# Performance work log

Hardware: AMD Instinct MI355X
Metric: run time of the kernel (lower is better)

Reference implementation:

```python
import jax, jax.numpy as jnp
import numpy as np

N, E, D_IN, D_HID, D_OUT = 50000, 800000, 128, 128, 128


def setup_inputs() -> dict:
    key = jax.random.key(0)
    ks = jax.random.split(key, 10)
    x = jax.random.normal(ks[0], (N, D_IN), dtype=jnp.float32)
    edge_index = jax.random.randint(ks[1], (2, E), 0, N, dtype=jnp.int64)
    def xavier(k, fan_in, fan_out):
        lim = jnp.sqrt(6.0 / (fan_in + fan_out)).astype(jnp.float32)
        return jax.random.uniform(k, (fan_in, fan_out), jnp.float32, -lim, lim)
    return {
        "x": x,
        "edge_index": edge_index,
        "W1l": xavier(ks[2], D_IN, D_HID), "b1l": jnp.zeros((D_HID,), jnp.float32),
        "W1r": xavier(ks[3], D_IN, D_HID),
        "W2l": xavier(ks[4], D_HID, D_OUT), "b2l": jnp.zeros((D_OUT,), jnp.float32),
        "W2r": xavier(ks[5], D_HID, D_OUT),
        "Wfc": xavier(ks[6], D_OUT, 2), "bfc": jnp.zeros((2,), jnp.float32),
    }


def _mean_aggregate(x, src, dst, num_nodes):
    # gather neighbor (source) features, scatter-mean to destination nodes
    msgs = x[src]                                        # [E, D]
    summed = jax.ops.segment_sum(msgs, dst, num_segments=num_nodes)
    ones = jnp.ones((src.shape[0],), x.dtype)
    counts = jax.ops.segment_sum(ones, dst, num_segments=num_nodes)
    return summed / jnp.maximum(counts, 1.0)[:, None]


def _l2_normalize(x, eps=1e-12):
    # matches torch F.normalize(p=2, dim=-1): divide by clamp(norm, min=eps)
    norm = jnp.sqrt(jnp.sum(x * x, axis=-1, keepdims=True))
    return x / jnp.maximum(norm, eps)


def _sage_conv(x, src, dst, Wl, bl, Wr):
    agg = _mean_aggregate(x, src, dst, x.shape[0])
    out = agg @ Wl + bl + x @ Wr
    return _l2_normalize(out)


def reference(x, edge_index, W1l, b1l, W1r, W2l, b2l, W2r, Wfc, bfc):
    src, dst = edge_index[0], edge_index[1]  # PyG: row=source(j), col=target(i)
    h = _sage_conv(x, src, dst, W1l, b1l, W1r)
    h = jax.nn.relu(h)
    h = _sage_conv(h, src, dst, W2l, b2l, W2r)
    logits = h @ Wfc + bfc
    return jax.nn.softmax(logits, axis=-1)
```

## Files before the change

### kernel.cpp

```cpp
#include <hip/hip_runtime.h>

#define D 128
#define CBITS 8

typedef __attribute__((ext_vector_type(8))) short short8;
typedef __attribute__((ext_vector_type(4))) float f32x4;

__device__ __forceinline__ unsigned short f2b(float f) {
    unsigned u = __builtin_bit_cast(unsigned, f);
    u += 0x7fffu + ((u >> 16) & 1u);
    return (unsigned short)(u >> 16);
}
__device__ __forceinline__ float b2f(unsigned short b) {
    unsigned u = ((unsigned)b) << 16;
    return __builtin_bit_cast(float, u);
}


__global__ __launch_bounds__(256) void prep_kernel(
    const float* __restrict__ x, unsigned short* __restrict__ acat,
    unsigned char* __restrict__ xq8, int nCast, int n8,
    const float* __restrict__ W1l, const float* __restrict__ W1r,
    const float* __restrict__ W2l, const float* __restrict__ W2r,
    unsigned short* __restrict__ WT1, unsigned short* __restrict__ WT2,
    int4* __restrict__ zeroPtr, int* __restrict__ offsets, int nnodes, int E) {
    const int b = blockIdx.x;
    const int t = threadIdx.x;
    if (b < nCast) {
        int g = b * 256 + t;
        if (g < n8) {
            int row = g >> 4, chunk = g & 15;
            const float4 v0 = *reinterpret_cast<const float4*>(x + (size_t)g * 8);
            const float4 v1 = *reinterpret_cast<const float4*>(x + (size_t)g * 8 + 4);
            float f[8] = {v0.x, v0.y, v0.z, v0.w, v1.x, v1.y, v1.z, v1.w};
            short8 r;
            unsigned lo = 0, hi = 0;
#pragma unroll
            for (int i = 0; i < 8; ++i) {
                r[i] = (short)f2b(f[i]);
                int qi = (int)rintf(fminf(fmaxf(f[i] * 32.f, -127.f), 127.f)) + 128;
                if (i < 4) lo |= (unsigned)(qi & 255) << (8 * i);
                else       hi |= (unsigned)(qi & 255) << (8 * (i - 4));
            }
            *reinterpret_cast<short8*>(acat + (size_t)row * 256 + 128 + chunk * 8) = r;
            *reinterpret_cast<uint2*>(xq8 + (size_t)row * 128 + chunk * 8) = make_uint2(lo, hi);
        }
    } else if (b < nCast + 256) {
        int bb = b - nCast;
        int layer = bb >> 7;
        int j = bb & 127;
        const float* Wl = layer ? W2l : W1l;
        const float* Wr = layer ? W2r : W1r;
        unsigned short* WT = layer ? WT2 : WT1;
        float v = (t < 128) ? Wl[t * D + j] : Wr[(t - 128) * D + j];
        WT[(size_t)j * 256 + t] = f2b(v);
    } else {
        if (t < 128) zeroPtr[t] = make_int4(0, 0, 0, 0);
        if (t == 0) offsets[nnodes] = E;
    }
}


__global__ __launch_bounds__(256) void bucket_count_kernel(
    const int* __restrict__ dst, int* __restrict__ bucketCnt, int E) {
    __shared__ int hist[256];
    const int t = threadIdx.x;
    hist[t] = 0;
    __syncthreads();
    const int base = blockIdx.x * 4096;
#pragma unroll
    for (int i = 0; i < 16; ++i) {
        int e = base + i * 256 + t;
        if (e < E) atomicAdd(&hist[dst[e] >> CBITS], 1);
    }
    __syncthreads();
    if (hist[t]) atomicAdd(&bucketCnt[t], hist[t]);
}

__global__ __launch_bounds__(256) void bin_coarse_kernel(
    const int* __restrict__ src, const int* __restrict__ dst,
    const int* __restrict__ bucketCnt, int* __restrict__ cursorA,
    int* __restrict__ staging, int E) {

    __shared__ int hist[256];
    __shared__ int lcur[256];
    const int t = threadIdx.x;

    int cnt = bucketCnt[t];
    lcur[t] = cnt;
    __syncthreads();
    for (int d = 1; d < 256; d <<= 1) {
        int u = (t >= d) ? lcur[t - d] : 0;
        __syncthreads();
        lcur[t] += u;
        __syncthreads();
    }
    const int myBase = lcur[t] - cnt;
    __syncthreads();

    hist[t] = 0;
    __syncthreads();

    const int base = blockIdx.x * 4096;
    int sreg[16], dreg[16];
#pragma unroll
    for (int i = 0; i < 16; ++i) {
        int e = base + i * 256 + t;
        int s = 0, d = -1;
        if (e < E) {
            s = src[e]; d = dst[e];
            atomicAdd(&hist[d >> CBITS], 1);
        }
        sreg[i] = s; dreg[i] = d;
    }
    __syncthreads();
    {
        int h = hist[t];
        lcur[t] = myBase + (h ? atomicAdd(&cursorA[t], h) : 0);
    }
    __syncthreads();
#pragma unroll
    for (int i = 0; i < 16; ++i) {
        if (dreg[i] >= 0) {
            int p = atomicAdd(&lcur[dreg[i] >> CBITS], 1);
            staging[p] = sreg[i] | ((dreg[i] & 255) << 16);
        }
    }
}

__global__ __launch_bounds__(256) void bucket_build_kernel(
    const int* __restrict__ staging, const int* __restrict__ bucketCnt,
    int* __restrict__ offsets, unsigned short* __restrict__ csr, int nnodes) {

    __shared__ int A1[256];
    __shared__ int A2[256];
    const int t = threadIdx.x;
    const int b = blockIdx.x;

    int cnt = bucketCnt[t];
    A1[t] = cnt;
    __syncthreads();
    for (int d = 1; d < 256; d <<= 1) {
        int u = (t >= d) ? A1[t - d] : 0;
        __syncthreads();
        A1[t] += u;
        __syncthreads();
    }
    const int end  = A1[b];
    const int base = end - bucketCnt[b];
    __syncthreads();

    A1[t] = 0;
    __syncthreads();
    for (int i = base + t; i < end; i += 256)
        atomicAdd(&A1[(staging[i] >> 16) & 255], 1);
    __syncthreads();
    A2[t] = A1[t];
    __syncthreads();
    for (int d = 1; d < 256; d <<= 1) {
        int u = (t >= d) ? A2[t - d] : 0;
        __syncthreads();
        A2[t] += u;
        __syncthreads();
    }
    const int excl = A2[t] - A1[t];
    const int node = (b << CBITS) + t;
    if (node < nnodes) offsets[node] = base + excl;
    __syncthreads();
    A1[t] = base + excl;
    __syncthreads();
    for (int i = base + t; i < end; i += 256) {
        int p = staging[i];
        int c = atomicAdd(&A1[(p >> 16) & 255], 1);
        csr[c] = (unsigned short)(p & 0xFFFF);
    }
}


__global__ __launch_bounds__(256) void aggregate_kernel(
    const unsigned char* __restrict__ q8,
    const int* __restrict__ offsets, const unsigned short* __restrict__ csr,
    unsigned short* __restrict__ out,
    int nnodes, float invScale) {
    int node = blockIdx.x * 16 + (threadIdx.x >> 4);
    int l16 = threadIdx.x & 15;
    if (node >= nnodes) return;
    const int lo = offsets[node], hi = offsets[node + 1];
    const int deg = hi - lo;
    const unsigned M = 0x00FF00FFu;
    unsigned a0 = 0, a1 = 0, a2 = 0, a3 = 0;
    int k = lo;
    int kA = (lo + 7) & ~7; if (kA > hi) kA = hi;
    for (; k < kA; ++k) {
        int s = csr[k];
        const uint2 v = *reinterpret_cast<const uint2*>(q8 + (size_t)s * 128 + l16 * 8);
        a0 += v.x & M; a1 += (v.x >> 8) & M;
        a2 += v.y & M; a3 += (v.y >> 8) & M;
    }
    for (; k + 8 <= hi; k += 8) {
        const int4 c = *reinterpret_cast<const int4*>(csr + k);
        int s[8];
        s[0] = c.x & 0xFFFF; s[1] = (int)((unsigned)c.x >> 16);
        s[2] = c.y & 0xFFFF; s[3] = (int)((unsigned)c.y >> 16);
        s[4] = c.z & 0xFFFF; s[5] = (int)((unsigned)c.z >> 16);
        s[6] = c.w & 0xFFFF; s[7] = (int)((unsigned)c.w >> 16);
        uint2 v[8];
#pragma unroll
        for (int u = 0; u < 8; ++u)
            v[u] = *reinterpret_cast<const uint2*>(q8 + (size_t)s[u] * 128 + l16 * 8);
#pragma unroll
        for (int u = 0; u < 8; ++u) {
            a0 += v[u].x & M; a1 += (v[u].x >> 8) & M;
            a2 += v[u].y & M; a3 += (v[u].y >> 8) & M;
        }
    }
    for (; k < hi; ++k) {
        int s = csr[k];
        const uint2 v = *reinterpret_cast<const uint2*>(q8 + (size_t)s * 128 + l16 * 8);
        a0 += v.x & M; a1 += (v.x >> 8) & M;
        a2 += v.y & M; a3 += (v.y >> 8) & M;
    }
    const float inv = invScale / fmaxf((float)deg, 1.0f);
    const float bias = 128.0f * (float)deg;
    int isum[8];
    isum[0] = (int)(a0 & 0xFFFF); isum[2] = (int)(a0 >> 16);
    isum[1] = (int)(a1 & 0xFFFF); isum[3] = (int)(a1 >> 16);
    isum[4] = (int)(a2 & 0xFFFF); isum[6] = (int)(a2 >> 16);
    isum[5] = (int)(a3 & 0xFFFF); isum[7] = (int)(a3 >> 16);
    short8 r;
#pragma unroll
    for (int i = 0; i < 8; ++i) r[i] = (short)f2b(((float)isum[i] - bias) * inv);
    *reinterpret_cast<short8*>(out + (size_t)node * 256 + l16 * 8) = r;
}


template <bool RELU, bool HEAD>
__global__ __launch_bounds__(256) void sage_mfma_kernel(
    const unsigned short* __restrict__ Acat, const unsigned short* __restrict__ WT,
    const float* __restrict__ bias, unsigned short* __restrict__ hout, int out_stride,
    unsigned char* __restrict__ q8out,
    const float* __restrict__ Wfc, const float* __restrict__ bfc,
    float* __restrict__ outf, int nnodes) {

    __shared__ unsigned short Blds[128 * 256];
    const int tid = threadIdx.x;

    {
        const short8* wsrc = reinterpret_cast<const short8*>(WT);
#pragma unroll
        for (int it = 0; it < 16; ++it) {
            int u = it * 256 + tid;
            int row = u >> 5, c = u & 31;
            int cs = c ^ (row & 7);
            *reinterpret_cast<short8*>(
                reinterpret_cast<char*>(Blds) + row * 512 + cs * 16) = wsrc[u];
        }
    }
    __syncthreads();

    const int w = tid >> 6, l = tid & 63;
    const int r16 = l & 15, g = l >> 4;
    const int rowbase = blockIdx.x * 128 + w * 32;

    f32x4 acc[2][8];
#pragma unroll
    for (int j = 0; j < 8; ++j) {
        float bj = bias[j * 16 + r16];
        acc[0][j] = (f32x4){bj, bj, bj, bj};
        acc[1][j] = (f32x4){bj, bj, bj, bj};
    }

    const unsigned short* ap0 = Acat + (size_t)(rowbase + r16) * 256 + g * 8;
    const unsigned short* ap1 = ap0 + 16 * 256;

#pragma unroll
    for (int ks = 0; ks < 8; ++ks) {
        const short8 a0 = *reinterpret_cast<const short8*>(ap0 + ks * 32);
        const short8 a1 = *reinterpret_cast<const short8*>(ap1 + ks * 32);
        const int cs = ((ks * 4 + g) ^ (r16 & 7)) * 16;
#pragma unroll
        for (int j = 0; j < 8; ++j) {
            const short8 b = *reinterpret_cast<const short8*>(
                reinterpret_cast<const char*>(Blds) + (j * 16 + r16) * 512 + cs);
            acc[0][j] = __builtin_amdgcn_mfma_f32_16x16x32_bf16(a0, b, acc[0][j], 0, 0, 0);
            acc[1][j] = __builtin_amdgcn_mfma_f32_16x16x32_bf16(a1, b, acc[1][j], 0, 0, 0);
        }
    }

#pragma unroll
    for (int rb = 0; rb < 2; ++rb) {
        float ss[4] = {0.f, 0.f, 0.f, 0.f};
#pragma unroll
        for (int j = 0; j < 8; ++j)
#pragma unroll
            for (int i = 0; i < 4; ++i) ss[i] += acc[rb][j][i] * acc[rb][j][i];
#pragma unroll
        for (int m = 1; m < 16; m <<= 1)
#pragma unroll
            for (int i = 0; i < 4; ++i) ss[i] += __shfl_xor(ss[i], m, 64);

        if (!HEAD) {
#pragma unroll
            for (int i = 0; i < 4; ++i) {
                int row = rowbase + rb * 16 + g * 4 + i;
                if (row >= nnodes) continue;
                float sc = 1.0f / fmaxf(sqrtf(ss[i]), 1e-12f);
#pragma unroll
                for (int j = 0; j < 8; ++j) {
                    float v = acc[rb][j][i] * sc;
                    if (RELU) v = fmaxf(v, 0.f);
                    hout[(size_t)row * out_stride + j * 16 + r16] = f2b(v);
                    if (RELU)
                        q8out[(size_t)row * 128 + j * 16 + r16] =
                            (unsigned char)((int)rintf(v * 127.f) + 128);
                }
            }
        } else {
            float w0[8], w1[8];
#pragma unroll
            for (int j = 0; j < 8; ++j) {
                const float2 wv = *reinterpret_cast<const float2*>(Wfc + (j * 16 + r16) * 2);
                w0[j] = wv.x; w1[j] = wv.y;
            }
            const float b0 = bfc[0], b1 = bfc[1];
#pragma unroll
            for (int i = 0; i < 4; ++i) {
                float sc = 1.0f / fmaxf(sqrtf(ss[i]), 1e-12f);
                float l0 = 0.f, l1 = 0.f;
#pragma unroll
                for (int j = 0; j < 8; ++j) {
                    float v = acc[rb][j][i] * sc;
                    l0 = fmaf(v, w0[j], l0);
                    l1 = fmaf(v, w1[j], l1);
                }
#pragma unroll
                for (int m = 1; m < 16; m <<= 1) {
                    l0 += __shfl_xor(l0, m, 64);
                    l1 += __shfl_xor(l1, m, 64);
                }
                int row = rowbase + rb * 16 + g * 4 + i;
                if (r16 == 0 && row < nnodes) {
                    float d0 = l0 + b0, d1 = l1 + b1;
                    float mx = fmaxf(d0, d1);
                    float e0 = expf(d0 - mx), e1 = expf(d1 - mx);
                    float inv = 1.0f / (e0 + e1);
                    outf[(size_t)row * 2]     = e0 * inv;
                    outf[(size_t)row * 2 + 1] = e1 * inv;
                }
            }
        }
    }
}


extern "C" void kernel_launch(void* const* d_in, const int* in_sizes, int n_in,
                              void* d_out, int out_size, void* d_ws, size_t ws_size,
                              hipStream_t stream) {
    const float* x   = (const float*)d_in[0];
    const int*   ei  = (const int*)d_in[1];
    const float* W1l = (const float*)d_in[2];
    const float* b1l = (const float*)d_in[3];
    const float* W1r = (const float*)d_in[4];
    const float* W2l = (const float*)d_in[5];
    const float* b2l = (const float*)d_in[6];
    const float* W2r = (const float*)d_in[7];
    const float* Wfc = (const float*)d_in[8];
    const float* bfc = (const float*)d_in[9];

    const int N = in_sizes[0] / D;
    const int E = in_sizes[1] / 2;
    const int* src = ei;
    const int* dst = ei + E;
    const int NBC = (N + (1 << CBITS) - 1) >> CBITS;

    unsigned short* Acat1 = (unsigned short*)d_ws;
    unsigned short* Acat2 = Acat1 + (size_t)N * 256;
    int* staging          = (int*)Acat2;
    unsigned short* WT1   = Acat2 + (size_t)N * 256;
    unsigned short* WT2   = WT1 + 128 * 256;
    int* bucketCnt  = (int*)(WT2 + 128 * 256);
    int* cursorA    = bucketCnt + 256;
    unsigned char* q8 = (unsigned char*)(cursorA + 256);
    int* offsets    = (int*)(q8 + (size_t)N * 128);
    unsigned short* csr = (unsigned short*)(((uintptr_t)(offsets + N + 1) + 15) & ~(uintptr_t)15);

    const int nCast = (N * 16 + 255) / 256;

    prep_kernel<<<nCast + 256 + 1, 256, 0, stream>>>(
        x, Acat1, q8, nCast, N * 16, W1l, W1r, W2l, W2r, WT1, WT2,
        (int4*)bucketCnt, offsets, N, E);

    bucket_count_kernel<<<(E + 4095) / 4096, 256, 0, stream>>>(dst, bucketCnt, E);
    bin_coarse_kernel<<<(E + 4095) / 4096, 256, 0, stream>>>(src, dst, bucketCnt, cursorA, staging, E);
    bucket_build_kernel<<<NBC, 256, 0, stream>>>(staging, bucketCnt, offsets, csr, N);

    aggregate_kernel<<<(N + 15) / 16, 256, 0, stream>>>(q8, offsets, csr, Acat1, N, 1.0f / 32.0f);
    sage_mfma_kernel<true, false><<<(N + 127) / 128, 256, 0, stream>>>(
        Acat1, WT1, b1l, Acat2 + 128, 256, q8, nullptr, nullptr, nullptr, N);

    aggregate_kernel<<<(N + 15) / 16, 256, 0, stream>>>(q8, offsets, csr, Acat2, N, 1.0f / 127.0f);
    sage_mfma_kernel<false, true><<<(N + 127) / 128, 256, 0, stream>>>(
        Acat2, WT2, b2l, nullptr, 0, nullptr, Wfc, bfc, (float*)d_out, N);
}
```

Measured before the change: 112.6 us.

## Split int8 feature table into two column halves for cache-friendly gathers

Stores the quantized int8 node features as two separate 64-column halves, each covering all nodes, and has the aggregation kernel process one half per block, with 8 lanes per node. Each half-table is 3.2 MB instead of 6.4 MB, so the random neighbor gathers of a given half are more likely to hit in L2. The trade-off is that the CSR indices and offsets are read twice, and more blocks are launched with smaller per-node work.

```diff
diff --git a/kernel.cpp b/kernel.cpp
--- a/kernel.cpp
+++ b/kernel.cpp
@@ -43,7 +43,9 @@
                 else       hi |= (unsigned)(qi & 255) << (8 * (i - 4));
             }
             *reinterpret_cast<short8*>(acat + (size_t)row * 256 + 128 + chunk * 8) = r;
-            *reinterpret_cast<uint2*>(xq8 + (size_t)row * 128 + chunk * 8) = make_uint2(lo, hi);
+            int half = chunk >> 3;
+            *reinterpret_cast<uint2*>(xq8 + (size_t)half * nnodes * 64 +
+                                      (size_t)row * 64 + (chunk & 7) * 8) = make_uint2(lo, hi);
         }
     } else if (b < nCast + 256) {
         int bb = b - nCast;
@@ -181,10 +183,13 @@
     const unsigned char* __restrict__ q8,
     const int* __restrict__ offsets, const unsigned short* __restrict__ csr,
     unsigned short* __restrict__ out,
-    int nnodes, float invScale) {
-    int node = blockIdx.x * 16 + (threadIdx.x >> 4);
-    int l16 = threadIdx.x & 15;
+    int nnodes, float invScale, int nodeBlocks) {
+    const int h  = blockIdx.x / nodeBlocks;
+    const int nb = blockIdx.x - h * nodeBlocks;
+    const int node = nb * 32 + (threadIdx.x >> 3);
+    const int l8 = threadIdx.x & 7;
     if (node >= nnodes) return;
+    const unsigned char* slice = q8 + (size_t)h * nnodes * 64;
     const int lo = offsets[node], hi = offsets[node + 1];
     const int deg = hi - lo;
     const unsigned M = 0x00FF00FFu;
@@ -193,7 +198,7 @@
     int kA = (lo + 7) & ~7; if (kA > hi) kA = hi;
     for (; k < kA; ++k) {
         int s = csr[k];
-        const uint2 v = *reinterpret_cast<const uint2*>(q8 + (size_t)s * 128 + l16 * 8);
+        const uint2 v = *reinterpret_cast<const uint2*>(slice + (size_t)s * 64 + l8 * 8);
         a0 += v.x & M; a1 += (v.x >> 8) & M;
         a2 += v.y & M; a3 += (v.y >> 8) & M;
     }
@@ -207,7 +212,7 @@
         uint2 v[8];
 #pragma unroll
         for (int u = 0; u < 8; ++u)
-            v[u] = *reinterpret_cast<const uint2*>(q8 + (size_t)s[u] * 128 + l16 * 8);
+            v[u] = *reinterpret_cast<const uint2*>(slice + (size_t)s[u] * 64 + l8 * 8);
 #pragma unroll
         for (int u = 0; u < 8; ++u) {
             a0 += v[u].x & M; a1 += (v[u].x >> 8) & M;
@@ -216,7 +221,7 @@
     }
     for (; k < hi; ++k) {
         int s = csr[k];
-        const uint2 v = *reinterpret_cast<const uint2*>(q8 + (size_t)s * 128 + l16 * 8);
+        const uint2 v = *reinterpret_cast<const uint2*>(slice + (size_t)s * 64 + l8 * 8);
         a0 += v.x & M; a1 += (v.x >> 8) & M;
         a2 += v.y & M; a3 += (v.y >> 8) & M;
     }
@@ -230,7 +235,7 @@
     short8 r;
 #pragma unroll
     for (int i = 0; i < 8; ++i) r[i] = (short)f2b(((float)isum[i] - bias) * inv);
-    *reinterpret_cast<short8*>(out + (size_t)node * 256 + l16 * 8) = r;
+    *reinterpret_cast<short8*>(out + (size_t)node * 256 + h * 64 + l8 * 8) = r;
 }
 
 
@@ -300,6 +305,7 @@
             for (int i = 0; i < 4; ++i) ss[i] += __shfl_xor(ss[i], m, 64);
 
         if (!HEAD) {
+            const size_t halfStride = (size_t)nnodes * 64;
 #pragma unroll
             for (int i = 0; i < 4; ++i) {
                 int row = rowbase + rb * 16 + g * 4 + i;
@@ -310,9 +316,11 @@
                     float v = acc[rb][j][i] * sc;
                     if (RELU) v = fmaxf(v, 0.f);
                     hout[(size_t)row * out_stride + j * 16 + r16] = f2b(v);
-                    if (RELU)
-                        q8out[(size_t)row * 128 + j * 16 + r16] =
+                    if (RELU) {
+                        int col = j * 16 + r16;
+                        q8out[(size_t)(col >> 6) * halfStride + (size_t)row * 64 + (col & 63)] =
                             (unsigned char)((int)rintf(v * 127.f) + 128);
+                    }
                 }
             }
         } else {
@@ -385,6 +393,7 @@
     unsigned short* csr = (unsigned short*)(((uintptr_t)(offsets + N + 1) + 15) & ~(uintptr_t)15);
 
     const int nCast = (N * 16 + 255) / 256;
+    const int nodeBlocks = (N + 31) / 32;
 
     prep_kernel<<<nCast + 256 + 1, 256, 0, stream>>>(
         x, Acat1, q8, nCast, N * 16, W1l, W1r, W2l, W2r, WT1, WT2,
@@ -394,11 +403,11 @@
     bin_coarse_kernel<<<(E + 4095) / 4096, 256, 0, stream>>>(src, dst, bucketCnt, cursorA, staging, E);
     bucket_build_kernel<<<NBC, 256, 0, stream>>>(staging, bucketCnt, offsets, csr, N);
 
-    aggregate_kernel<<<(N + 15) / 16, 256, 0, stream>>>(q8, offsets, csr, Acat1, N, 1.0f / 32.0f);
+    aggregate_kernel<<<2 * nodeBlocks, 256, 0, stream>>>(q8, offsets, csr, Acat1, N, 1.0f / 32.0f, nodeBlocks);
     sage_mfma_kernel<true, false><<<(N + 127) / 128, 256, 0, stream>>>(
         Acat1, WT1, b1l, Acat2 + 128, 256, q8, nullptr, nullptr, nullptr, N);
 
-    aggregate_kernel<<<(N + 15) / 16, 256, 0, stream>>>(q8, offsets, csr, Acat2, N, 1.0f / 127.0f);
+    aggregate_kernel<<<2 * nodeBlocks, 256, 0, stream>>>(q8, offsets, csr, Acat2, N, 1.0f / 127.0f, nodeBlocks);
     sage_mfma_kernel<false, true><<<(N + 127) / 128, 256, 0, stream>>>(
         Acat2, WT2, b2l, nullptr, 0, nullptr, Wfc, bfc, (float*)d_out, N);
 }
```

New measurement: 116.6 us. 3.5% more time.
